# Performance work log

Hardware: AMD Instinct MI355X
Metric: run time of the kernel (lower is better)

## Reference

```python
import jax, jax.numpy as jnp
import numpy as np

HEADS = 8
DIM_HEAD = 64
ROPE_THETA = 10000.0


def setup_inputs() -> dict:
    key = jax.random.key(0)
    ks = jax.random.split(key, 6)
    b, hw, n, dim = 2, 1024, 32, 512
    hidden = HEADS * DIM_HEAD
    x = jax.random.normal(ks[0], (b, hw, n, dim), jnp.float32)
    pos_bias = jax.random.normal(ks[1], (HEADS, n, n), jnp.float32)
    w_q = jax.random.normal(ks[2], (dim, hidden), jnp.float32) * 0.02
    w_kv = jax.random.normal(ks[3], (dim, 2 * hidden), jnp.float32) * 0.02
    w_out = jax.random.normal(ks[4], (hidden, dim), jnp.float32) * 0.02
    inv_freq = 1.0 / (ROPE_THETA ** (jnp.arange(0, DIM_HEAD, 2, dtype=jnp.float32) / DIM_HEAD))
    focus_present_mask = jax.random.randint(ks[5], (b,), 0, 2) > 0  # mixed True/False
    return dict(x=x, pos_bias=pos_bias, focus_present_mask=focus_present_mask,
                w_q=w_q, w_kv=w_kv, w_out=w_out, inv_freq=inv_freq)


def _rope(t, inv_freq):
    # rotary-embedding-torch default: interleaved pairs over full head dim
    n, d = t.shape[-2], t.shape[-1]
    pos = jnp.arange(n, dtype=inv_freq.dtype)
    freqs = pos[:, None] * inv_freq[None, :]          # (n, d/2)
    freqs = jnp.repeat(freqs, 2, axis=-1)             # (n, d) interleaved
    cos, sin = jnp.cos(freqs), jnp.sin(freqs)
    tp = t.reshape(*t.shape[:-1], d // 2, 2)
    t_rot = jnp.stack((-tp[..., 1], tp[..., 0]), axis=-1).reshape(t.shape)
    return t * cos + t_rot * sin


def _split_heads(t):
    # ... n (h d) -> ... h n d
    t = t.reshape(*t.shape[:-1], HEADS, DIM_HEAD)
    return jnp.moveaxis(t, -2, -3)


def reference(x, pos_bias, focus_present_mask, w_q, w_kv, w_out, inv_freq):
    n = x.shape[-2]
    q = x @ w_q                                        # (b, s, n, hidden)
    k, v = jnp.split(x @ w_kv, 2, axis=-1)
    q, k, v = map(_split_heads, (q, k, v))             # (b, s, h, n, d)
    q = q * (DIM_HEAD ** -0.5)
    q = _rope(q, inv_freq)
    k = _rope(k, inv_freq)
    sim = jnp.einsum('...hid,...hjd->...hij', q, k) + pos_bias  # (b, s, h, n, n)
    # focus-present mask: batches with True attend only to self (diag), others attend all
    eye = jnp.eye(n, dtype=bool)
    mask = jnp.where(focus_present_mask[:, None, None, None, None], eye, True)
    sim = jnp.where(mask, sim, -jnp.finfo(sim.dtype).max)
    m = jax.lax.stop_gradient(jnp.max(sim, axis=-1, keepdims=True))
    e = jnp.exp(sim - m)
    attn = e / jnp.sum(e, axis=-1, keepdims=True)
    out = jnp.einsum('...hij,...hjd->...hid', attn, v)  # (b, s, h, n, d)
    out = jnp.moveaxis(out, -3, -2).reshape(*x.shape[:-1], HEADS * DIM_HEAD)
    return out @ w_out
```

## Files before the change

### kernel.cpp

```cpp
#include <hip/hip_runtime.h>
#include <hip/hip_bf16.h>
#include <stdint.h>


typedef __attribute__((ext_vector_type(8))) short short8;
typedef __attribute__((ext_vector_type(4))) float f32x4;
typedef __attribute__((ext_vector_type(4))) unsigned int u32x4;

#define GPTR(p) ((const __attribute__((address_space(1))) void*)(p))
#define SPTR(p) ((__attribute__((address_space(3))) void*)(p))

__device__ __forceinline__ float b2f(unsigned short h) {
  union { unsigned u; float f; } c; c.u = ((unsigned)h) << 16; return c.f;
}
__device__ __forceinline__ unsigned short f2b(float f) {
  union { float f; unsigned u; } c; c.f = f;
  unsigned u = c.u;
  return (unsigned short)((u + 0x7fffu + ((u >> 16) & 1u)) >> 16);
}

__device__ __forceinline__ bool get_mask(const void* p, int b) {
  const unsigned* u = (const unsigned*)p;
  unsigned v0 = u[0], v1 = u[1];
  if (v0 <= 1u && v1 <= 1u) return (b ? v1 : v0) != 0u;
  const unsigned char* c = (const unsigned char*)p;
  return c[b] != 0;
}

__global__ __launch_bounds__(256) void prep(
    const float* __restrict__ wq, const float* __restrict__ wkv,
    const float* __restrict__ wout, const float* __restrict__ invf,
    unsigned short* __restrict__ W1t, unsigned short* __restrict__ W2t,
    float* __restrict__ cos_t, float* __restrict__ sin_t) {
  const int tid = blockIdx.x * 256 + threadIdx.x;
  if (tid < 1536 * 512) {
    const int j = tid >> 9, kk = tid & 511;
    float v = (j < 512) ? wq[kk * 512 + j] * 0.125f : wkv[kk * 1024 + (j - 512)];
    W1t[tid] = f2b(v);
  }
  if (tid < 512 * 512) {
    const int j = tid >> 9, kk = tid & 511;
    W2t[tid] = f2b(wout[kk * 512 + j]);
  }
  if (tid < 1024) {
    const int i = tid >> 5, p = tid & 31;
    const float f = (float)i * invf[p];
    cos_t[tid] = cosf(f);
    sin_t[tid] = sinf(f);
  }
}

__global__ __launch_bounds__(256) void convert_x(const float* __restrict__ x,
                                                 unsigned short* __restrict__ xb) {
  const int i = (blockIdx.x * 256 + threadIdx.x) * 8;
  const float4 a = *(const float4*)(x + i);
  const float4 b = *(const float4*)(x + i + 4);
  union { unsigned short us[8]; u32x4 v; } o;
  o.us[0] = f2b(a.x); o.us[1] = f2b(a.y); o.us[2] = f2b(a.z); o.us[3] = f2b(a.w);
  o.us[4] = f2b(b.x); o.us[5] = f2b(b.y); o.us[6] = f2b(b.z); o.us[7] = f2b(b.w);
  *(u32x4*)(xb + i) = o.v;
}

template <int OUT_MODE>
__global__ __launch_bounds__(256, 2) void gemm_bt(
    const unsigned short* __restrict__ A, const unsigned short* __restrict__ Bt,
    void* __restrict__ Cout, int M, int N, int K) {
  __shared__ __align__(16) unsigned short smem[17408];
  unsigned short* As = smem;
  unsigned short* Bs = smem + 8192;

  const int nb = N >> 7;
  const int cpx = gridDim.x >> 3;
  const int bid = (blockIdx.x & 7) * cpx + (blockIdx.x >> 3);
  const int bm = bid / nb, bn = bid % nb;
  const int t = threadIdx.x, lane = t & 63, w = t >> 6;
  const int wm = (w >> 1) << 6, wn = (w & 1) << 6;

  f32x4 acc[4][4] = {};

  const size_t Ks = (size_t)K;
  const unsigned short* gA = A + (size_t)(bm * 128 + w * 32 + (lane >> 3)) * Ks + ((lane & 7) << 3);
  const unsigned short* gB = Bt + (size_t)(bn * 128 + w * 32 + (lane >> 3)) * Ks + ((lane & 7) << 3);
  unsigned short* lA = As + w * 32 * 64;
  unsigned short* lB = Bs + w * 32 * 64;

  for (int k0 = 0; k0 < K; k0 += 64) {
#pragma unroll
    for (int i = 0; i < 4; ++i) {
      __builtin_amdgcn_global_load_lds(GPTR(gA + (size_t)i * 8 * Ks), SPTR(lA + i * 512), 16, 0, 0);
      __builtin_amdgcn_global_load_lds(GPTR(gB + (size_t)i * 8 * Ks), SPTR(lB + i * 512), 16, 0, 0);
    }
    gA += 64; gB += 64;
    __syncthreads();
#pragma unroll
    for (int ks = 0; ks < 2; ++ks) {
      const int kr = (ks << 5) + ((lane >> 4) << 3);
      const int r = lane & 15;
      short8 af[4], bf[4];
#pragma unroll
      for (int x = 0; x < 4; ++x) af[x] = *(const short8*)(As + (wm + (x << 4) + r) * 64 + kr);
#pragma unroll
      for (int x = 0; x < 4; ++x) bf[x] = *(const short8*)(Bs + (wn + (x << 4) + r) * 64 + kr);
#pragma unroll
      for (int xm = 0; xm < 4; ++xm)
#pragma unroll
        for (int xn = 0; xn < 4; ++xn)
          acc[xm][xn] = __builtin_amdgcn_mfma_f32_16x16x32_bf16(af[xm], bf[xn], acc[xm][xn], 0, 0, 0);
    }
    __syncthreads();
  }

  if (OUT_MODE == 0) {
    unsigned short* Ct = smem;
    const int cb = wn + (lane & 15);
    const int rb = wm + ((lane >> 4) << 2);
#pragma unroll
    for (int xn = 0; xn < 4; ++xn)
#pragma unroll
      for (int xm = 0; xm < 4; ++xm) {
        const f32x4 v = acc[xm][xn];
        unsigned long long pk = (unsigned long long)f2b(v[0]) |
                                ((unsigned long long)f2b(v[1]) << 16) |
                                ((unsigned long long)f2b(v[2]) << 32) |
                                ((unsigned long long)f2b(v[3]) << 48);
        *(unsigned long long*)(Ct + (size_t)(cb + (xn << 4)) * 136 + rb + (xm << 4)) = pk;
      }
    __syncthreads();
    unsigned short* Cg = (unsigned short*)Cout;
#pragma unroll
    for (int it = 0; it < 8; ++it) {
      const int idx = it * 256 + t;
      const int c = idx >> 4;
      const int rc = (idx & 15) << 3;
      const u32x4 val = *(const u32x4*)(Ct + c * 136 + rc);
      *(u32x4*)(Cg + (size_t)(bn * 128 + c) * (size_t)M + (size_t)bm * 128 + rc) = val;
    }
  } else {
    float* Cg = (float*)Cout;
    const int cb = bn * 128 + wn + (lane & 15);
    const int rb = bm * 128 + wm + ((lane >> 4) << 2);
#pragma unroll
    for (int xm = 0; xm < 4; ++xm)
#pragma unroll
      for (int xn = 0; xn < 4; ++xn)
#pragma unroll
        for (int u = 0; u < 4; ++u)
          Cg[(size_t)(rb + (xm << 4) + u) * (size_t)N + cb + (xn << 4)] = acc[xm][xn][u];
  }
}

__global__ __launch_bounds__(256, 2) void gemm_qk(
    const unsigned short* __restrict__ A, const unsigned short* __restrict__ Bt,
    unsigned short* __restrict__ qkout,
    const float* __restrict__ cos_t, const float* __restrict__ sin_t) {
  __shared__ __align__(16) unsigned short smem[17408];
  unsigned short* As = smem;
  unsigned short* Bs = smem + 8192;

  const int K = 512;
  const int bid = (blockIdx.x & 7) * 512 + (blockIdx.x >> 3);
  const int bm = bid >> 3, bn = bid & 7;
  const int t = threadIdx.x, lane = t & 63, w = t >> 6;
  const int wm = (w >> 1) << 6, wn = (w & 1) << 6;
  const int l15 = lane & 15, l4 = lane >> 4;

  f32x4 acc[4][4] = {};

  const size_t Ks = (size_t)K;
  const unsigned short* gA = A + (size_t)(bm * 128 + w * 32 + (lane >> 3)) * Ks + ((lane & 7) << 3);
  const unsigned short* gB = Bt + (size_t)(bn * 128 + w * 32 + (lane >> 3)) * Ks + ((lane & 7) << 3);
  unsigned short* lA = As + w * 32 * 64;
  unsigned short* lB = Bs + w * 32 * 64;

  for (int k0 = 0; k0 < K; k0 += 64) {
#pragma unroll
    for (int i = 0; i < 4; ++i) {
      __builtin_amdgcn_global_load_lds(GPTR(gA + (size_t)i * 8 * Ks), SPTR(lA + i * 512), 16, 0, 0);
      __builtin_amdgcn_global_load_lds(GPTR(gB + (size_t)i * 8 * Ks), SPTR(lB + i * 512), 16, 0, 0);
    }
    gA += 64; gB += 64;
    __syncthreads();
#pragma unroll
    for (int ks = 0; ks < 2; ++ks) {
      const int kr = (ks << 5) + (l4 << 3);
      short8 af[4], bf[4];
#pragma unroll
      for (int x = 0; x < 4; ++x) af[x] = *(const short8*)(As + (wm + (x << 4) + l15) * 64 + kr);
#pragma unroll
      for (int x = 0; x < 4; ++x) bf[x] = *(const short8*)(Bs + (wn + (x << 4) + l15) * 64 + kr);
#pragma unroll
      for (int xn = 0; xn < 4; ++xn)
#pragma unroll
        for (int xm = 0; xm < 4; ++xm)
          acc[xn][xm] = __builtin_amdgcn_mfma_f32_16x16x32_bf16(bf[xn], af[xm], acc[xn][xm], 0, 0, 0);
    }
    __syncthreads();
  }

  unsigned short* Ct = smem;
#pragma unroll
  for (int xn = 0; xn < 4; ++xn)
#pragma unroll
    for (int xm = 0; xm < 4; ++xm) {
      const int tloc = wm + (xm << 4) + l15;
      const int pos = tloc & 31;
      const int nloc = wn + (xn << 4) + (l4 << 2);
      const int p0 = ((bn * 128 + nloc) >> 1) & 31;
      const float c0 = cos_t[pos * 32 + p0], s0 = sin_t[pos * 32 + p0];
      const float c1 = cos_t[pos * 32 + p0 + 1], s1 = sin_t[pos * 32 + p0 + 1];
      const f32x4 v = acc[xn][xm];
      const float o0 = v[0] * c0 - v[1] * s0;
      const float o1 = v[1] * c0 + v[0] * s0;
      const float o2 = v[2] * c1 - v[3] * s1;
      const float o3 = v[3] * c1 + v[2] * s1;
      unsigned long long pk = (unsigned long long)f2b(o0) |
                              ((unsigned long long)f2b(o1) << 16) |
                              ((unsigned long long)f2b(o2) << 32) |
                              ((unsigned long long)f2b(o3) << 48);
      *(unsigned long long*)(Ct + (size_t)tloc * 136 + nloc) = pk;
    }
  __syncthreads();
#pragma unroll
  for (int it = 0; it < 8; ++it) {
    const int idx = it * 256 + t;
    const int tok = idx >> 4;
    const int c8 = (idx & 15) << 3;
    const u32x4 val = *(const u32x4*)(Ct + tok * 136 + c8);
    *(u32x4*)(qkout + (size_t)(bm * 128 + tok) * 1024 + bn * 128 + c8) = val;
  }
}

__global__ __launch_bounds__(256) void attn2(
    const unsigned short* __restrict__ qk,
    const unsigned short* __restrict__ vbuf,
    const float* __restrict__ pos_bias,
    const void* __restrict__ maskp,
    unsigned short* __restrict__ attn_out) {
  const int wv = threadIdx.x >> 6;
  const int lane = threadIdx.x & 63;
  const int unit = blockIdx.x * 4 + wv;
  const int bs = unit >> 3, h = unit & 7;
  const int row0 = bs << 5;
  const int l15 = lane & 15, l4 = lane >> 4;

  __shared__ __align__(16) char lds[4 * 6656];
  char* wb = lds + wv * 6656;
  float* S = (float*)wb;
  unsigned short* Olds = (unsigned short*)wb;
  unsigned short* Pp = (unsigned short*)(wb + 4608);

  const unsigned short* qb = qk + (size_t)row0 * 1024 + h * 64;
  short8 qf[2][2], kf[2][2];
#pragma unroll
  for (int ti = 0; ti < 2; ++ti)
#pragma unroll
    for (int ks = 0; ks < 2; ++ks) {
      const size_t off = (size_t)((ti << 4) + l15) * 1024 + (ks << 5) + (l4 << 3);
      qf[ti][ks] = *(const short8*)(qb + off);
      kf[ti][ks] = *(const short8*)(qb + 512 + off);
    }
  f32x4 sc[2][2];
#pragma unroll
  for (int ti = 0; ti < 2; ++ti)
#pragma unroll
    for (int tj = 0; tj < 2; ++tj) {
      f32x4 z = {0.f, 0.f, 0.f, 0.f};
      z = __builtin_amdgcn_mfma_f32_16x16x32_bf16(qf[ti][0], kf[tj][0], z, 0, 0, 0);
      sc[ti][tj] = __builtin_amdgcn_mfma_f32_16x16x32_bf16(qf[ti][1], kf[tj][1], z, 0, 0, 0);
    }
#pragma unroll
  for (int ti = 0; ti < 2; ++ti)
#pragma unroll
    for (int tj = 0; tj < 2; ++tj)
#pragma unroll
      for (int r = 0; r < 4; ++r)
        S[((ti << 4) + (l4 << 2) + r) * 36 + (tj << 4) + l15] = sc[ti][tj][r];
  __syncthreads();

  {
    const int i = lane & 31;
    const int c = lane >> 5;
    const bool fm = get_mask(maskp, bs >> 10);
    float v[16];
    const float* Sr = S + i * 36 + (c << 4);
    const float* bp = pos_bias + h * 1024 + i * 32 + (c << 4);
#pragma unroll
    for (int g = 0; g < 4; ++g) {
      const float4 sv = *(const float4*)(Sr + (g << 2));
      const float4 bv = *(const float4*)(bp + (g << 2));
      v[g * 4 + 0] = sv.x + bv.x; v[g * 4 + 1] = sv.y + bv.y;
      v[g * 4 + 2] = sv.z + bv.z; v[g * 4 + 3] = sv.w + bv.w;
    }
    float m = v[0];
#pragma unroll
    for (int j = 1; j < 16; ++j) m = fmaxf(m, v[j]);
    m = fmaxf(m, __shfl_xor(m, 32, 64));
    float sum = 0.f;
#pragma unroll
    for (int j = 0; j < 16; ++j) { v[j] = __expf(v[j] - m); sum += v[j]; }
    sum += __shfl_xor(sum, 32, 64);
    const float inv = 1.f / sum;
    union { unsigned short us[8]; u32x4 u; } w0, w1;
    if (fm) {
#pragma unroll
      for (int j = 0; j < 8; ++j) {
        w0.us[j] = (((c << 4) + j) == i) ? (unsigned short)0x3F80 : (unsigned short)0;
        w1.us[j] = (((c << 4) + 8 + j) == i) ? (unsigned short)0x3F80 : (unsigned short)0;
      }
    } else {
#pragma unroll
      for (int j = 0; j < 8; ++j) {
        w0.us[j] = f2b(v[j] * inv);
        w1.us[j] = f2b(v[8 + j] * inv);
      }
    }
    const int ti = i >> 4, i15 = i & 15;
    *(u32x4*)(Pp + (size_t)((ti << 6) + ((2 * c + 0) << 4) + i15) * 8) = w0.u;
    *(u32x4*)(Pp + (size_t)((ti << 6) + ((2 * c + 1) << 4) + i15) * 8) = w1.u;
  }
  __syncthreads();

  short8 pf[2];
#pragma unroll
  for (int ti = 0; ti < 2; ++ti) pf[ti] = *(const short8*)(Pp + (size_t)((ti << 6) + lane) * 8);
  short8 vf[4];
#pragma unroll
  for (int td = 0; td < 4; ++td)
    vf[td] = *(const short8*)(vbuf + (size_t)(h * 64 + (td << 4) + l15) * 65536 + row0 + (l4 << 3));
  f32x4 o[2][4];
#pragma unroll
  for (int ti = 0; ti < 2; ++ti)
#pragma unroll
    for (int td = 0; td < 4; ++td) {
      f32x4 z = {0.f, 0.f, 0.f, 0.f};
      o[ti][td] = __builtin_amdgcn_mfma_f32_16x16x32_bf16(pf[ti], vf[td], z, 0, 0, 0);
    }
  __syncthreads();

#pragma unroll
  for (int ti = 0; ti < 2; ++ti)
#pragma unroll
    for (int td = 0; td < 4; ++td)
#pragma unroll
      for (int r = 0; r < 4; ++r)
        Olds[((ti << 4) + (l4 << 2) + r) * 72 + (td << 4) + l15] = f2b(o[ti][td][r]);
  __syncthreads();
#pragma unroll
  for (int p = 0; p < 4; ++p) {
    const int idx = (p << 6) + lane;
    const int i = idx >> 3;
    const int ch = (idx & 7) << 3;
    const u32x4 val = *(const u32x4*)(Olds + i * 72 + ch);
    *(u32x4*)(attn_out + (size_t)(row0 + i) * 512 + h * 64 + ch) = val;
  }
}

extern "C" void kernel_launch(void* const* d_in, const int* in_sizes, int n_in,
                              void* d_out, int out_size, void* d_ws, size_t ws_size,
                              hipStream_t stream) {
  const float* x = (const float*)d_in[0];
  const float* pos_bias = (const float*)d_in[1];
  const void* maskp = d_in[2];
  const float* wq = (const float*)d_in[3];
  const float* wkv = (const float*)d_in[4];
  const float* wout = (const float*)d_in[5];
  const float* invf = (const float*)d_in[6];

  char* ws = (char*)d_ws;
  unsigned short* xb = (unsigned short*)(ws);
  unsigned short* qkbuf = (unsigned short*)(ws + 67108864);
  unsigned short* vbuf = (unsigned short*)(ws + 201326592);
  unsigned short* W1t = (unsigned short*)(ws + 268435456);
  unsigned short* W2t = (unsigned short*)(ws + 270008320);
  float* cos_t = (float*)(ws + 270532608);
  float* sin_t = (float*)(ws + 270536704);

  prep<<<3072, 256, 0, stream>>>(wq, wkv, wout, invf, W1t, W2t, cos_t, sin_t);
  convert_x<<<16384, 256, 0, stream>>>(x, xb);
  gemm_qk<<<4096, 256, 0, stream>>>(xb, W1t, qkbuf, cos_t, sin_t);
  gemm_bt<0><<<2048, 256, 0, stream>>>(xb, W1t + (size_t)1024 * 512, (void*)vbuf, 65536, 512, 512);
  attn2<<<4096, 256, 0, stream>>>(qkbuf, vbuf, pos_bias, maskp, xb);
  gemm_bt<1><<<2048, 256, 0, stream>>>(xb, W2t, d_out, 65536, 512, 512);
}
```

Baseline: 547.5 us.

## Rewrite QK projection GEMM as 256x256 tile with multi-stage LDS ring pipeline

Replaces the 128x128 QK GEMM with a 256x256-tile, 512-thread kernel. It streams K in 32-wide slices through an 8-slot LDS ring using async global-to-LDS loads, explicit vmcnt waits and barriers, an XOR swizzle against bank conflicts, and setprio around the MFMA bursts. The goal is to overlap global loads with MFMA compute and raise arithmetic intensity per loaded byte. In exchange it needs more registers and more complex barrier scheduling, and the RoPE epilogue is split into two passes through LDS.

```diff
diff --git a/kernel.cpp b/kernel.cpp
--- a/kernel.cpp
+++ b/kernel.cpp
@@ -149,84 +149,142 @@
   }
 }
 
-__global__ __launch_bounds__(256, 2) void gemm_qk(
-    const unsigned short* __restrict__ A, const unsigned short* __restrict__ Bt,
+template <int TT, int WQ, int SSLOT, int SMAT, bool DOSTG, int VMN>
+__device__ __forceinline__ void phase256(
+    const unsigned short* __restrict__ gA, const unsigned short* __restrict__ gB,
+    unsigned short (&ring)[8][256][32], f32x4 (&acc)[8][4], short8 (&bf)[4],
+    int w, int wm, int wn, int l15, int l4, int koff) {
+  constexpr int KH = WQ >> 1;
+  constexpr int G = WQ & 1;
+  constexpr int SA = TT * 4 + KH * 2;
+  constexpr int SB = SA + 1;
+  short8 af[4];
+#pragma unroll
+  for (int x = 0; x < 4; ++x) {
+    const int row = wm * 128 + (G * 4 + x) * 16 + l15;
+    af[x] = *(const short8*)(&ring[SA][row][(l4 ^ (row & 3)) << 3]);
+  }
+  if constexpr (G == 0) {
+#pragma unroll
+    for (int x = 0; x < 4; ++x) {
+      const int row = wn * 64 + x * 16 + l15;
+      bf[x] = *(const short8*)(&ring[SB][row][(l4 ^ (row & 3)) << 3]);
+    }
+  }
+  if constexpr (DOSTG) {
+    const unsigned short* src = (SMAT ? gB : gA) + koff;
+#pragma unroll
+    for (int i = 0; i < 2; ++i)
+      __builtin_amdgcn_global_load_lds(GPTR(src + (size_t)i * 16 * 512),
+                                       SPTR(&ring[SSLOT][w * 32 + i * 16][0]), 16, 0, 0);
+  }
+  __builtin_amdgcn_s_barrier();
+  asm volatile("" ::: "memory");
+  __builtin_amdgcn_s_setprio(1);
+#pragma unroll
+  for (int x = 0; x < 4; ++x)
+#pragma unroll
+    for (int n = 0; n < 4; ++n)
+      acc[G * 4 + x][n] =
+          __builtin_amdgcn_mfma_f32_16x16x32_bf16(bf[n], af[x], acc[G * 4 + x][n], 0, 0, 0);
+  __builtin_amdgcn_s_setprio(0);
+  if constexpr (VMN == 8) asm volatile("s_waitcnt vmcnt(8)" ::: "memory");
+  if constexpr (VMN == 4) asm volatile("s_waitcnt vmcnt(4)" ::: "memory");
+  if constexpr (VMN == 0) asm volatile("s_waitcnt vmcnt(0)" ::: "memory");
+  __builtin_amdgcn_s_barrier();
+  asm volatile("" ::: "memory");
+}
+
+__global__ __launch_bounds__(512, 2) void gemm_qk256(
+    const unsigned short* __restrict__ A,
+    const unsigned short* __restrict__ Bt,
     unsigned short* __restrict__ qkout,
     const float* __restrict__ cos_t, const float* __restrict__ sin_t) {
-  __shared__ __align__(16) unsigned short smem[17408];
-  unsigned short* As = smem;
-  unsigned short* Bs = smem + 8192;
-
-  const int K = 512;
-  const int bid = (blockIdx.x & 7) * 512 + (blockIdx.x >> 3);
-  const int bm = bid >> 3, bn = bid & 7;
+  __shared__ __align__(16) unsigned short ring[8][256][32];
+
+  const int bid = ((blockIdx.x & 7) << 7) + (blockIdx.x >> 3);
+  const int bm = bid >> 2, bn = bid & 3;
   const int t = threadIdx.x, lane = t & 63, w = t >> 6;
-  const int wm = (w >> 1) << 6, wn = (w & 1) << 6;
+  const int wm = w >> 2, wn = w & 3;
   const int l15 = lane & 15, l4 = lane >> 4;
 
-  f32x4 acc[4][4] = {};
-
-  const size_t Ks = (size_t)K;
-  const unsigned short* gA = A + (size_t)(bm * 128 + w * 32 + (lane >> 3)) * Ks + ((lane & 7) << 3);
-  const unsigned short* gB = Bt + (size_t)(bn * 128 + w * 32 + (lane >> 3)) * Ks + ((lane & 7) << 3);
-  unsigned short* lA = As + w * 32 * 64;
-  unsigned short* lB = Bs + w * 32 * 64;
-
-  for (int k0 = 0; k0 < K; k0 += 64) {
-#pragma unroll
-    for (int i = 0; i < 4; ++i) {
-      __builtin_amdgcn_global_load_lds(GPTR(gA + (size_t)i * 8 * Ks), SPTR(lA + i * 512), 16, 0, 0);
-      __builtin_amdgcn_global_load_lds(GPTR(gB + (size_t)i * 8 * Ks), SPTR(lB + i * 512), 16, 0, 0);
-    }
-    gA += 64; gB += 64;
+  const int swz = ((lane & 3) ^ ((lane >> 2) & 3)) << 3;
+  const unsigned short* gA = A + (size_t)(bm * 256 + w * 32 + (lane >> 2)) * 512 + swz;
+  const unsigned short* gB = Bt + (size_t)(bn * 256 + w * 32 + (lane >> 2)) * 512 + swz;
+
+  f32x4 acc[8][4] = {};
+  short8 bf[4];
+
+#pragma unroll
+  for (int h = 0; h < 6; ++h) {
+    const unsigned short* src = ((h & 1) ? gB : gA) + (h >> 1) * 32;
+#pragma unroll
+    for (int i = 0; i < 2; ++i)
+      __builtin_amdgcn_global_load_lds(GPTR(src + (size_t)i * 16 * 512),
+                                       SPTR(&ring[h][w * 32 + i * 16][0]), 16, 0, 0);
+  }
+  asm volatile("s_waitcnt vmcnt(8)" ::: "memory");
+  __builtin_amdgcn_s_barrier();
+  asm volatile("" ::: "memory");
+
+  for (int it = 0; it < 3; ++it) {
+    const int kb = it * 128;
+    phase256<0, 0, 6, 0, true, -1>(gA, gB, ring, acc, bf, w, wm, wn, l15, l4, kb + 96);
+    phase256<0, 1, 7, 1, true, 8>(gA, gB, ring, acc, bf, w, wm, wn, l15, l4, kb + 96);
+    phase256<0, 2, 0, 0, true, -1>(gA, gB, ring, acc, bf, w, wm, wn, l15, l4, kb + 128);
+    phase256<0, 3, 1, 1, true, 8>(gA, gB, ring, acc, bf, w, wm, wn, l15, l4, kb + 128);
+    phase256<1, 0, 2, 0, true, -1>(gA, gB, ring, acc, bf, w, wm, wn, l15, l4, kb + 160);
+    phase256<1, 1, 3, 1, true, 8>(gA, gB, ring, acc, bf, w, wm, wn, l15, l4, kb + 160);
+    phase256<1, 2, 4, 0, true, -1>(gA, gB, ring, acc, bf, w, wm, wn, l15, l4, kb + 192);
+    phase256<1, 3, 5, 1, true, 8>(gA, gB, ring, acc, bf, w, wm, wn, l15, l4, kb + 192);
+  }
+  phase256<0, 0, 6, 0, true, -1>(gA, gB, ring, acc, bf, w, wm, wn, l15, l4, 480);
+  phase256<0, 1, 7, 1, true, 8>(gA, gB, ring, acc, bf, w, wm, wn, l15, l4, 480);
+  phase256<0, 2, 0, 0, false, -1>(gA, gB, ring, acc, bf, w, wm, wn, l15, l4, 0);
+  phase256<0, 3, 1, 1, false, 4>(gA, gB, ring, acc, bf, w, wm, wn, l15, l4, 0);
+  phase256<1, 0, 2, 0, false, -1>(gA, gB, ring, acc, bf, w, wm, wn, l15, l4, 0);
+  phase256<1, 1, 3, 1, false, 0>(gA, gB, ring, acc, bf, w, wm, wn, l15, l4, 0);
+  phase256<1, 2, 4, 0, false, -1>(gA, gB, ring, acc, bf, w, wm, wn, l15, l4, 0);
+  phase256<1, 3, 5, 1, false, -1>(gA, gB, ring, acc, bf, w, wm, wn, l15, l4, 0);
+
+  unsigned short* Ct = &ring[0][0][0];
+#pragma unroll
+  for (int p = 0; p < 2; ++p) {
+    if ((wn >> 1) == p) {
+#pragma unroll
+      for (int mt = 0; mt < 8; ++mt) {
+        const int t_loc = wm * 128 + mt * 16 + l15;
+        const int pos = t_loc & 31;
+#pragma unroll
+        for (int nt = 0; nt < 4; ++nt) {
+          const int f_loc = wn * 64 + nt * 16 + (l4 << 2);
+          const int p0 = (f_loc >> 1) & 31;
+          const float c0 = cos_t[pos * 32 + p0], s0 = sin_t[pos * 32 + p0];
+          const float c1 = cos_t[pos * 32 + p0 + 1], s1 = sin_t[pos * 32 + p0 + 1];
+          const f32x4 v = acc[mt][nt];
+          const float o0 = v[0] * c0 - v[1] * s0;
+          const float o1 = v[1] * c0 + v[0] * s0;
+          const float o2 = v[2] * c1 - v[3] * s1;
+          const float o3 = v[3] * c1 + v[2] * s1;
+          unsigned long long pk = (unsigned long long)f2b(o0) |
+                                  ((unsigned long long)f2b(o1) << 16) |
+                                  ((unsigned long long)f2b(o2) << 32) |
+                                  ((unsigned long long)f2b(o3) << 48);
+          const int c_loc = (wn & 1) * 64 + nt * 16 + (l4 << 2);
+          *(unsigned long long*)(Ct + (size_t)t_loc * 132 + c_loc) = pk;
+        }
+      }
+    }
     __syncthreads();
 #pragma unroll
-    for (int ks = 0; ks < 2; ++ks) {
-      const int kr = (ks << 5) + (l4 << 3);
-      short8 af[4], bf[4];
-#pragma unroll
-      for (int x = 0; x < 4; ++x) af[x] = *(const short8*)(As + (wm + (x << 4) + l15) * 64 + kr);
-#pragma unroll
-      for (int x = 0; x < 4; ++x) bf[x] = *(const short8*)(Bs + (wn + (x << 4) + l15) * 64 + kr);
-#pragma unroll
-      for (int xn = 0; xn < 4; ++xn)
-#pragma unroll
-        for (int xm = 0; xm < 4; ++xm)
-          acc[xn][xm] = __builtin_amdgcn_mfma_f32_16x16x32_bf16(bf[xn], af[xm], acc[xn][xm], 0, 0, 0);
+    for (int itst = 0; itst < 8; ++itst) {
+      const int idx = itst * 512 + t;
+      const int row = idx >> 4;
+      const int c8 = (idx & 15) << 3;
+      const u32x4 val = *(const u32x4*)(Ct + row * 132 + c8);
+      *(u32x4*)(qkout + (size_t)(bm * 256 + row) * 1024 + bn * 256 + p * 128 + c8) = val;
     }
     __syncthreads();
-  }
-
-  unsigned short* Ct = smem;
-#pragma unroll
-  for (int xn = 0; xn < 4; ++xn)
-#pragma unroll
-    for (int xm = 0; xm < 4; ++xm) {
-      const int tloc = wm + (xm << 4) + l15;
-      const int pos = tloc & 31;
-      const int nloc = wn + (xn << 4) + (l4 << 2);
-      const int p0 = ((bn * 128 + nloc) >> 1) & 31;
-      const float c0 = cos_t[pos * 32 + p0], s0 = sin_t[pos * 32 + p0];
-      const float c1 = cos_t[pos * 32 + p0 + 1], s1 = sin_t[pos * 32 + p0 + 1];
-      const f32x4 v = acc[xn][xm];
-      const float o0 = v[0] * c0 - v[1] * s0;
-      const float o1 = v[1] * c0 + v[0] * s0;
-      const float o2 = v[2] * c1 - v[3] * s1;
-      const float o3 = v[3] * c1 + v[2] * s1;
-      unsigned long long pk = (unsigned long long)f2b(o0) |
-                              ((unsigned long long)f2b(o1) << 16) |
-                              ((unsigned long long)f2b(o2) << 32) |
-                              ((unsigned long long)f2b(o3) << 48);
-      *(unsigned long long*)(Ct + (size_t)tloc * 136 + nloc) = pk;
-    }
-  __syncthreads();
-#pragma unroll
-  for (int it = 0; it < 8; ++it) {
-    const int idx = it * 256 + t;
-    const int tok = idx >> 4;
-    const int c8 = (idx & 15) << 3;
-    const u32x4 val = *(const u32x4*)(Ct + tok * 136 + c8);
-    *(u32x4*)(qkout + (size_t)(bm * 128 + tok) * 1024 + bn * 128 + c8) = val;
   }
 }
 
@@ -377,7 +435,7 @@
 
   prep<<<3072, 256, 0, stream>>>(wq, wkv, wout, invf, W1t, W2t, cos_t, sin_t);
   convert_x<<<16384, 256, 0, stream>>>(x, xb);
-  gemm_qk<<<4096, 256, 0, stream>>>(xb, W1t, qkbuf, cos_t, sin_t);
+  gemm_qk256<<<1024, 512, 0, stream>>>(xb, W1t, qkbuf, cos_t, sin_t);
   gemm_bt<0><<<2048, 256, 0, stream>>>(xb, W1t + (size_t)1024 * 512, (void*)vbuf, 65536, 512, 512);
   attn2<<<4096, 256, 0, stream>>>(qkbuf, vbuf, pos_bias, maskp, xb);
   gemm_bt<1><<<2048, 256, 0, stream>>>(xb, W2t, d_out, 65536, 512, 512);
```

Result: no change. 555.7 us (+1.5%).

## Fuse output projection into attention kernel with one block per token group

Applied to the files above, without the earlier changes.

Attention is restructured so each 512-thread block handles all 8 heads of one 32-token group. The per-head outputs are gathered in LDS as a 32x512 bf16 tile, and the block then multiplies it by W_out with MFMA, writing fp32 output directly. This drops the separate output GEMM launch and the bf16 round trip of the attention output through global memory. In exchange every block rereads the full W_out from global/L2 without LDS staging, and the final stores are scattered 4-byte writes rather than vectorized ones.

```diff
diff --git a/kernel.cpp b/kernel.cpp
--- a/kernel.cpp
+++ b/kernel.cpp
@@ -230,24 +230,24 @@
   }
 }
 
-__global__ __launch_bounds__(256) void attn2(
+__global__ __launch_bounds__(512, 4) void attn3(
     const unsigned short* __restrict__ qk,
     const unsigned short* __restrict__ vbuf,
     const float* __restrict__ pos_bias,
     const void* __restrict__ maskp,
-    unsigned short* __restrict__ attn_out) {
-  const int wv = threadIdx.x >> 6;
+    const unsigned short* __restrict__ W2t,
+    float* __restrict__ out) {
+  const int h = threadIdx.x >> 6;
   const int lane = threadIdx.x & 63;
-  const int unit = blockIdx.x * 4 + wv;
-  const int bs = unit >> 3, h = unit & 7;
+  const int bs = blockIdx.x;
   const int row0 = bs << 5;
   const int l15 = lane & 15, l4 = lane >> 4;
 
-  __shared__ __align__(16) char lds[4 * 6656];
-  char* wb = lds + wv * 6656;
+  __shared__ __align__(16) char lds[8 * 6656];
+  char* wb = lds + h * 6656;
   float* S = (float*)wb;
-  unsigned short* Olds = (unsigned short*)wb;
   unsigned short* Pp = (unsigned short*)(wb + 4608);
+  unsigned short* OldsB = (unsigned short*)lds;
 
   const unsigned short* qb = qk + (size_t)row0 * 1024 + h * 64;
   short8 qf[2][2], kf[2][2];
@@ -343,16 +343,36 @@
     for (int td = 0; td < 4; ++td)
 #pragma unroll
       for (int r = 0; r < 4; ++r)
-        Olds[((ti << 4) + (l4 << 2) + r) * 72 + (td << 4) + l15] = f2b(o[ti][td][r]);
+        OldsB[((ti << 4) + (l4 << 2) + r) * 520 + (h << 6) + (td << 4) + l15] =
+            f2b(o[ti][td][r]);
   __syncthreads();
-#pragma unroll
-  for (int p = 0; p < 4; ++p) {
-    const int idx = (p << 6) + lane;
-    const int i = idx >> 3;
-    const int ch = (idx & 7) << 3;
-    const u32x4 val = *(const u32x4*)(Olds + i * 72 + ch);
-    *(u32x4*)(attn_out + (size_t)(row0 + i) * 512 + h * 64 + ch) = val;
-  }
+
+  f32x4 pacc[2][4] = {};
+  const unsigned short* Wp = W2t + (size_t)(h << 6) * 512;
+#pragma unroll
+  for (int ks = 0; ks < 16; ++ks) {
+    const int kr = (ks << 5) + (l4 << 3);
+    short8 af0 = *(const short8*)(OldsB + (size_t)l15 * 520 + kr);
+    short8 af1 = *(const short8*)(OldsB + (size_t)(16 + l15) * 520 + kr);
+    short8 bfr[4];
+#pragma unroll
+    for (int x = 0; x < 4; ++x)
+      bfr[x] = *(const short8*)(Wp + (size_t)((x << 4) + l15) * 512 + kr);
+#pragma unroll
+    for (int n = 0; n < 4; ++n) {
+      pacc[0][n] = __builtin_amdgcn_mfma_f32_16x16x32_bf16(af0, bfr[n], pacc[0][n], 0, 0, 0);
+      pacc[1][n] = __builtin_amdgcn_mfma_f32_16x16x32_bf16(af1, bfr[n], pacc[1][n], 0, 0, 0);
+    }
+  }
+  const int cb = (h << 6) + l15;
+  const int rb = l4 << 2;
+#pragma unroll
+  for (int m = 0; m < 2; ++m)
+#pragma unroll
+    for (int n = 0; n < 4; ++n)
+#pragma unroll
+      for (int u = 0; u < 4; ++u)
+        out[(size_t)(row0 + (m << 4) + rb + u) * 512 + cb + (n << 4)] = pacc[m][n][u];
 }
 
 extern "C" void kernel_launch(void* const* d_in, const int* in_sizes, int n_in,
@@ -379,6 +399,5 @@
   convert_x<<<16384, 256, 0, stream>>>(x, xb);
   gemm_qk<<<4096, 256, 0, stream>>>(xb, W1t, qkbuf, cos_t, sin_t);
   gemm_bt<0><<<2048, 256, 0, stream>>>(xb, W1t + (size_t)1024 * 512, (void*)vbuf, 65536, 512, 512);
-  attn2<<<4096, 256, 0, stream>>>(qkbuf, vbuf, pos_bias, maskp, xb);
-  gemm_bt<1><<<2048, 256, 0, stream>>>(xb, W2t, d_out, 65536, 512, 512);
-}
+  attn3<<<2048, 512, 0, stream>>>(qkbuf, vbuf, pos_bias, maskp, W2t, (float*)d_out);
+}
```

Result: slower. 596.2 us (+8.9%).

## Double-buffer LDS tiles in projection GEMMs to overlap loads with MFMA

Applied to the files above, without the earlier changes.

Both GEMM kernels (gemm_bt and the RoPE-fused gemm_qk) now use two LDS stages. The next K-tile is issued with global_load_lds into the alternate buffer right after the barrier, while MFMAs run on the current buffer. This aims to hide global-to-LDS latency and removes the second barrier per iteration. In exchange the LDS footprint per block doubles to 64KB, which may limit occupancy, and correctness relies on the barrier's implicit wait for outstanding DMA loads.

```diff
diff --git a/kernel.cpp b/kernel.cpp
--- a/kernel.cpp
+++ b/kernel.cpp
@@ -65,9 +65,7 @@
 __global__ __launch_bounds__(256, 2) void gemm_bt(
     const unsigned short* __restrict__ A, const unsigned short* __restrict__ Bt,
     void* __restrict__ Cout, int M, int N, int K) {
-  __shared__ __align__(16) unsigned short smem[17408];
-  unsigned short* As = smem;
-  unsigned short* Bs = smem + 8192;
+  __shared__ __align__(16) unsigned short smem[32768];
 
   const int nb = N >> 7;
   const int cpx = gridDim.x >> 3;
@@ -81,17 +79,29 @@
   const size_t Ks = (size_t)K;
   const unsigned short* gA = A + (size_t)(bm * 128 + w * 32 + (lane >> 3)) * Ks + ((lane & 7) << 3);
   const unsigned short* gB = Bt + (size_t)(bn * 128 + w * 32 + (lane >> 3)) * Ks + ((lane & 7) << 3);
-  unsigned short* lA = As + w * 32 * 64;
-  unsigned short* lB = Bs + w * 32 * 64;
-
-  for (int k0 = 0; k0 < K; k0 += 64) {
-#pragma unroll
-    for (int i = 0; i < 4; ++i) {
-      __builtin_amdgcn_global_load_lds(GPTR(gA + (size_t)i * 8 * Ks), SPTR(lA + i * 512), 16, 0, 0);
-      __builtin_amdgcn_global_load_lds(GPTR(gB + (size_t)i * 8 * Ks), SPTR(lB + i * 512), 16, 0, 0);
-    }
-    gA += 64; gB += 64;
+  const int lofs = w * 32 * 64;
+
+  const int kiter = K >> 6;
+#pragma unroll
+  for (int i = 0; i < 4; ++i) {
+    __builtin_amdgcn_global_load_lds(GPTR(gA + (size_t)i * 8 * Ks), SPTR(smem + lofs + i * 512), 16, 0, 0);
+    __builtin_amdgcn_global_load_lds(GPTR(gB + (size_t)i * 8 * Ks), SPTR(smem + 8192 + lofs + i * 512), 16, 0, 0);
+  }
+  gA += 64; gB += 64;
+
+  for (int it = 0; it < kiter; ++it) {
     __syncthreads();
+    if (it + 1 < kiter) {
+      unsigned short* dst = smem + ((it + 1) & 1) * 16384;
+#pragma unroll
+      for (int i = 0; i < 4; ++i) {
+        __builtin_amdgcn_global_load_lds(GPTR(gA + (size_t)i * 8 * Ks), SPTR(dst + lofs + i * 512), 16, 0, 0);
+        __builtin_amdgcn_global_load_lds(GPTR(gB + (size_t)i * 8 * Ks), SPTR(dst + 8192 + lofs + i * 512), 16, 0, 0);
+      }
+      gA += 64; gB += 64;
+    }
+    const unsigned short* As = smem + (it & 1) * 16384;
+    const unsigned short* Bs = As + 8192;
 #pragma unroll
     for (int ks = 0; ks < 2; ++ks) {
       const int kr = (ks << 5) + ((lane >> 4) << 3);
@@ -107,8 +117,8 @@
         for (int xn = 0; xn < 4; ++xn)
           acc[xm][xn] = __builtin_amdgcn_mfma_f32_16x16x32_bf16(af[xm], bf[xn], acc[xm][xn], 0, 0, 0);
     }
-    __syncthreads();
-  }
+  }
+  __syncthreads();
 
   if (OUT_MODE == 0) {
     unsigned short* Ct = smem;
@@ -153,9 +163,7 @@
     const unsigned short* __restrict__ A, const unsigned short* __restrict__ Bt,
     unsigned short* __restrict__ qkout,
     const float* __restrict__ cos_t, const float* __restrict__ sin_t) {
-  __shared__ __align__(16) unsigned short smem[17408];
-  unsigned short* As = smem;
-  unsigned short* Bs = smem + 8192;
+  __shared__ __align__(16) unsigned short smem[32768];
 
   const int K = 512;
   const int bid = (blockIdx.x & 7) * 512 + (blockIdx.x >> 3);
@@ -169,17 +177,28 @@
   const size_t Ks = (size_t)K;
   const unsigned short* gA = A + (size_t)(bm * 128 + w * 32 + (lane >> 3)) * Ks + ((lane & 7) << 3);
   const unsigned short* gB = Bt + (size_t)(bn * 128 + w * 32 + (lane >> 3)) * Ks + ((lane & 7) << 3);
-  unsigned short* lA = As + w * 32 * 64;
-  unsigned short* lB = Bs + w * 32 * 64;
-
-  for (int k0 = 0; k0 < K; k0 += 64) {
-#pragma unroll
-    for (int i = 0; i < 4; ++i) {
-      __builtin_amdgcn_global_load_lds(GPTR(gA + (size_t)i * 8 * Ks), SPTR(lA + i * 512), 16, 0, 0);
-      __builtin_amdgcn_global_load_lds(GPTR(gB + (size_t)i * 8 * Ks), SPTR(lB + i * 512), 16, 0, 0);
-    }
-    gA += 64; gB += 64;
+  const int lofs = w * 32 * 64;
+
+#pragma unroll
+  for (int i = 0; i < 4; ++i) {
+    __builtin_amdgcn_global_load_lds(GPTR(gA + (size_t)i * 8 * Ks), SPTR(smem + lofs + i * 512), 16, 0, 0);
+    __builtin_amdgcn_global_load_lds(GPTR(gB + (size_t)i * 8 * Ks), SPTR(smem + 8192 + lofs + i * 512), 16, 0, 0);
+  }
+  gA += 64; gB += 64;
+
+  for (int it = 0; it < 8; ++it) {
     __syncthreads();
+    if (it + 1 < 8) {
+      unsigned short* dst = smem + ((it + 1) & 1) * 16384;
+#pragma unroll
+      for (int i = 0; i < 4; ++i) {
+        __builtin_amdgcn_global_load_lds(GPTR(gA + (size_t)i * 8 * Ks), SPTR(dst + lofs + i * 512), 16, 0, 0);
+        __builtin_amdgcn_global_load_lds(GPTR(gB + (size_t)i * 8 * Ks), SPTR(dst + 8192 + lofs + i * 512), 16, 0, 0);
+      }
+      gA += 64; gB += 64;
+    }
+    const unsigned short* As = smem + (it & 1) * 16384;
+    const unsigned short* Bs = As + 8192;
 #pragma unroll
     for (int ks = 0; ks < 2; ++ks) {
       const int kr = (ks << 5) + (l4 << 3);
@@ -194,8 +213,8 @@
         for (int xm = 0; xm < 4; ++xm)
           acc[xn][xm] = __builtin_amdgcn_mfma_f32_16x16x32_bf16(bf[xn], af[xm], acc[xn][xm], 0, 0, 0);
     }
-    __syncthreads();
-  }
+  }
+  __syncthreads();
 
   unsigned short* Ct = smem;
 #pragma unroll
```

Measured after the change: 537.9 us. Within noise of the previous version (-1.8%).
